# Kernel tuning notes

Measured on AMD Instinct MI355X. Metric: run time of the kernel, lower is better.

The kernel has to match this reference:

```python
import jax, jax.numpy as jnp
import numpy as np

B, T = 2048, 512
H1, H2, H3 = 100, 60, 30


def _glorot(key, shape, fan):
    bound = 1.0 / np.sqrt(fan)
    return jax.random.uniform(key, shape, jnp.float32, -bound, bound)


def setup_inputs() -> dict:
    key = jax.random.key(0)
    ks = jax.random.split(key, 17)
    inp = {"x": jax.random.normal(ks[0], (B, T, 2), jnp.float32)}
    # layer 1: input 2 -> hidden 100
    inp["W_ih1"] = _glorot(ks[1], (H1, 2), H1)
    inp["W_hh1"] = _glorot(ks[2], (H1, H1), H1)
    inp["b_ih1"] = _glorot(ks[3], (H1,), H1)
    inp["b_hh1"] = _glorot(ks[4], (H1,), H1)
    # layer 2: 100 -> 60
    inp["W_ih2"] = _glorot(ks[5], (H2, H1), H2)
    inp["W_hh2"] = _glorot(ks[6], (H2, H2), H2)
    inp["b_ih2"] = _glorot(ks[7], (H2,), H2)
    inp["b_hh2"] = _glorot(ks[8], (H2,), H2)
    # layer 3: 60 -> 30
    inp["W_ih3"] = _glorot(ks[9], (H3, H2), H3)
    inp["W_hh3"] = _glorot(ks[10], (H3, H3), H3)
    inp["b_ih3"] = _glorot(ks[11], (H3,), H3)
    inp["b_hh3"] = _glorot(ks[12], (H3,), H3)
    # heads
    inp["W_o1"] = _glorot(ks[13], (10, H3), 10)
    inp["b_o1"] = _glorot(ks[14], (10,), 10)
    inp["W_o2"] = _glorot(ks[15], (2, 10), 2)
    inp["b_o2"] = _glorot(ks[16], (2,), 2)
    return inp


def rnn_layer(x, W_ih, W_hh, b_ih, b_hh):
    # x: [B, T, in]; precompute the time-parallel input projection once
    xp = jnp.einsum("bti,hi->bth", x, W_ih) + (b_ih + b_hh)  # [B, T, H]
    h0 = jnp.zeros((x.shape[0], W_hh.shape[0]), x.dtype)

    def step(h, xt):  # xt: [B, H]
        h = jnp.tanh(xt + h @ W_hh.T)
        return h, h

    _, ys = jax.lax.scan(step, h0, jnp.swapaxes(xp, 0, 1))  # [T, B, H]
    return jnp.swapaxes(ys, 0, 1)  # [B, T, H]


def reference(x, W_ih1, W_hh1, b_ih1, b_hh1, W_ih2, W_hh2, b_ih2, b_hh2,
              W_ih3, W_hh3, b_ih3, b_hh3, W_o1, b_o1, W_o2, b_o2):
    h = rnn_layer(x, W_ih1, W_hh1, b_ih1, b_hh1)
    h = rnn_layer(h, W_ih2, W_hh2, b_ih2, b_hh2)
    h = rnn_layer(h, W_ih3, W_hh3, b_ih3, b_hh3)
    o = jnp.einsum("bth,oh->bto", h, W_o1) + b_o1
    return jnp.einsum("bto,po->btp", o, W_o2) + b_o2  # [B, T, 2]
```

## Files before the change

### kernel.cpp

```cpp
#include <hip/hip_runtime.h>

typedef _Float16 v8hf __attribute__((ext_vector_type(8)));
typedef float    v4f  __attribute__((ext_vector_type(4)));

#define MFMA16(a, b, c) __builtin_amdgcn_mfma_f32_16x16x32_f16((a), (b), (c), 0, 0, 0)

#define TT 512
#define BT 16
#define NTH 512
#define KS 2.8853900817779268f
#define CL 13.8498724f

#define H1R 0u
#define H2R 8192u
#define XST 12288u
#define ORG 45120u

__shared__ __align__(16) char SM[53312];

__device__ __forceinline__ v4f tanh4s(v4f z) {
    float z0 = __builtin_amdgcn_fmed3f(z[0], -CL, CL);
    float z1 = __builtin_amdgcn_fmed3f(z[1], -CL, CL);
    float z2 = __builtin_amdgcn_fmed3f(z[2], -CL, CL);
    float z3 = __builtin_amdgcn_fmed3f(z[3], -CL, CL);
    float a0 = __builtin_amdgcn_exp2f(z0) + 1.f;
    float a1 = __builtin_amdgcn_exp2f(z1) + 1.f;
    float a2 = __builtin_amdgcn_exp2f(z2) + 1.f;
    float a3 = __builtin_amdgcn_exp2f(z3) + 1.f;
    float P = a0 * a1, Q = a2 * a3;
    float R = __builtin_amdgcn_rcpf(P * Q);
    float iP = Q * R, iQ = P * R;
    v4f t;
    t[0] = 1.f - 2.f * (a1 * iP);
    t[1] = 1.f - 2.f * (a0 * iP);
    t[2] = 1.f - 2.f * (a3 * iQ);
    t[3] = 1.f - 2.f * (a2 * iQ);
    return t;
}

__device__ __forceinline__ unsigned pk2h(float a, float b) {
    union { _Float16 h[2]; unsigned u; } x;
    x.h[0] = (_Float16)a; x.h[1] = (_Float16)b;
    return x.u;
}
__device__ __forceinline__ v8hf mk8(unsigned a, unsigned b, unsigned c, unsigned d) {
    union { unsigned u[4]; v8hf h; } x;
    x.u[0] = a; x.u[1] = b; x.u[2] = c; x.u[3] = d;
    return x.h;
}

__global__ __launch_bounds__(NTH, 1)
void rnn3_sw(const float* __restrict__ xg,
             const float* __restrict__ Wih1, const float* __restrict__ Whh1,
             const float* __restrict__ bih1, const float* __restrict__ bhh1,
             const float* __restrict__ Wih2, const float* __restrict__ Whh2,
             const float* __restrict__ bih2, const float* __restrict__ bhh2,
             const float* __restrict__ Wih3, const float* __restrict__ Whh3,
             const float* __restrict__ bih3, const float* __restrict__ bhh3,
             const float* __restrict__ Wo1,  const float* __restrict__ bo1,
             const float* __restrict__ Wo2,  const float* __restrict__ bo2,
             float* __restrict__ outg)
{
    const int tid   = threadIdx.x;
    const int lane  = tid & 63;
    const int wid   = tid >> 6;
    const int col   = lane & 15;
    const int g     = lane >> 4;
    const int bbase = blockIdx.x * BT;
    const unsigned l16 = (unsigned)lane * 16u;

    {
        float4 z = {0.f, 0.f, 0.f, 0.f};
        for (int i = tid; i < 768; i += NTH) ((float4*)SM)[i] = z;
        for (int i = tid; i < BT * TT; i += NTH) {
            const int b = i >> 9, t = i & 511;
            float2 xv = *(const float2*)(xg + (size_t)(bbase + b) * (TT * 2) + 2 * t);
            *(unsigned*)(SM + XST + (unsigned)t * 64u + (unsigned)b * 4u) = pk2h(xv.x, xv.y);
        }
        if (tid < 16) *(unsigned*)(SM + XST + 512u * 64u + (unsigned)tid * 4u) = 0u;
    }

    v8hf WF[12];
    #pragma unroll
    for (int i = 0; i < 12; ++i) WF[i] = (v8hf)(_Float16)0.f;
    v4f BB0 = {0.f,0.f,0.f,0.f}, BB1 = {0.f,0.f,0.f,0.f}, BH = {0.f,0.f,0.f,0.f};
    v8hf ST = (v8hf)(_Float16)0.f;

    auto ldA = [&](const float* W, int rows, int cols, int jg, int kt) -> v8hf {
        v8hf r;
        #pragma unroll
        for (int e = 0; e < 8; ++e) {
            const int kl = 32 * kt + 16 * (e >> 2) + 4 * g + (e & 3);
            float v = (jg < rows && kl < cols) ? W[jg * cols + kl] * KS : 0.f;
            r[e] = (_Float16)v;
        }
        return r;
    };
    auto ldA1 = [&](int jg, int kt) -> v8hf {
        v8hf r;
        #pragma unroll
        for (int e = 0; e < 8; ++e) {
            const int kl = 32 * kt + 16 * (e >> 2) + 4 * g + (e & 3);
            float v = 0.f;
            if (jg < 100) {
                if (kl < 100)       v = Whh1[jg * 100 + kl];
                else if (kl == 112) v = Wih1[jg * 2];
                else if (kl == 113) v = Wih1[jg * 2 + 1];
            }
            r[e] = (_Float16)(v * KS);
        }
        return r;
    };
    auto mkbias = [&](const float* bi, const float* bh, int n, int t) -> v4f {
        v4f b;
        #pragma unroll
        for (int i = 0; i < 4; ++i) {
            const int j = 16 * t + 4 * g + i;
            b[i] = (j < n) ? KS * (bi[j] + bh[j]) : 0.f;
        }
        return b;
    };

    if (wid < 3) {
        const int tA = 2 * wid;
        #pragma unroll
        for (int kt = 0; kt < 4; ++kt) {
            WF[kt]     = ldA1(16 * tA + col, kt);
            WF[4 + kt] = ldA1(16 * tA + 16 + col, kt);
        }
        BB0 = mkbias(bih1, bhh1, 100, tA);
        BB1 = mkbias(bih1, bhh1, 100, tA + 1);
    } else if (wid == 3) {
        #pragma unroll
        for (int kt = 0; kt < 4; ++kt) WF[kt] = ldA1(96 + col, kt);
        BB0 = mkbias(bih1, bhh1, 100, 6);
    } else if (wid < 6) {
        const int tA = 2 * (wid - 4);
        #pragma unroll
        for (int kt = 0; kt < 4; ++kt) {
            WF[kt]     = ldA(Wih2, 60, 100, 16 * tA + col, kt);
            WF[4 + kt] = ldA(Wih2, 60, 100, 16 * tA + 16 + col, kt);
        }
        WF[8]  = ldA(Whh2, 60, 60, 16 * tA + col, 0);
        WF[9]  = ldA(Whh2, 60, 60, 16 * tA + col, 1);
        WF[10] = ldA(Whh2, 60, 60, 16 * tA + 16 + col, 0);
        WF[11] = ldA(Whh2, 60, 60, 16 * tA + 16 + col, 1);
        BB0 = mkbias(bih2, bhh2, 60, tA);
        BB1 = mkbias(bih2, bhh2, 60, tA + 1);
    } else if (wid == 6) {
        WF[0] = ldA(Wih3, 30, 60, col, 0);       WF[1] = ldA(Wih3, 30, 60, col, 1);
        WF[2] = ldA(Wih3, 30, 60, col + 16, 0);  WF[3] = ldA(Wih3, 30, 60, col + 16, 1);
        WF[4] = ldA(Whh3, 30, 30, col, 0);       WF[5] = ldA(Whh3, 30, 30, col + 16, 0);
        #pragma unroll
        for (int e = 0; e < 8; ++e) {
            const int kl = 16 * (e >> 2) + 4 * g + (e & 3);
            float v = 0.f;
            if (col < 2 && kl < 30) {
                #pragma unroll
                for (int u = 0; u < 10; ++u) v += Wo2[col * 10 + u] * Wo1[u * 30 + kl];
            }
            WF[6][e] = (_Float16)v;
        }
        BB0 = mkbias(bih3, bhh3, 30, 0);
        BB1 = mkbias(bih3, bhh3, 30, 1);
        #pragma unroll
        for (int i = 0; i < 4; ++i) {
            float bv = 0.f;
            if (g == 0 && i < 2) {
                bv = bo2[i];
                #pragma unroll
                for (int u = 0; u < 10; ++u) bv += Wo2[i * 10 + u] * bo1[u];
            }
            BH[i] = bv;
        }
    }

    __syncthreads();
    if (tid < 16)
        *(unsigned*)(SM + H1R + 4096u + 3072u + (unsigned)tid * 16u + 8u) =
            *(const unsigned*)(SM + XST + (unsigned)tid * 4u);
    if (wid == 3) {
        unsigned x0 = *(const unsigned*)(SM + XST + (unsigned)col * 4u);
        ST = mk8(0u, 0u, (g == 0) ? x0 : 0u, 0u);
    }
    __syncthreads();

    auto flushfn = [&](int tbase) {
        const unsigned rb = ORG + (((unsigned)tbase & 63u) >> 1) * 16u;
        #pragma unroll
        for (int jj = 0; jj < 4; ++jj) {
            const int f = lane + 64 * jj;
            const int b = f >> 4, k = f & 15;
            float4 v = *(const float4*)(SM + rb + (unsigned)b * 512u + (unsigned)k * 16u);
            *(float4*)(outg + ((size_t)(bbase + b) * TT + tbase) * 2 + 4 * k) = v;
        }
    };

    unsigned rO1 = H1R + 4096u, wO1 = H1R;
    unsigned rO2 = H2R + 2048u, wO2 = H2R;
    const v4f z4 = {0.f, 0.f, 0.f, 0.f};

    for (int s = 0; s < TT + 2; ++s) {
        if (wid == 0) {
            if (s < TT) {
                v8hf S1 = *(const v8hf*)(SM + rO1 + 1024u + l16);
                v8hf S2 = *(const v8hf*)(SM + rO1 + 2048u + l16);
                v8hf S3 = *(const v8hf*)(SM + rO1 + 3072u + l16);
                v4f p = BB0, q = z4;
                p = MFMA16(WF[0], ST, p); q = MFMA16(WF[1], S1, q);
                p = MFMA16(WF[2], S2, p); q = MFMA16(WF[3], S3, q);
                v4f r0 = tanh4s(p + q);
                p = BB1; q = z4;
                p = MFMA16(WF[4], ST, p); q = MFMA16(WF[5], S1, q);
                p = MFMA16(WF[6], S2, p); q = MFMA16(WF[7], S3, q);
                v4f r1 = tanh4s(p + q);
                ST = mk8(pk2h(r0[0], r0[1]), pk2h(r0[2], r0[3]),
                         pk2h(r1[0], r1[1]), pk2h(r1[2], r1[3]));
                *(v8hf*)(SM + wO1 + l16) = ST;
            }
        } else if (wid == 1) {
            if (s < TT) {
                v8hf S0 = *(const v8hf*)(SM + rO1 + l16);
                v8hf S2 = *(const v8hf*)(SM + rO1 + 2048u + l16);
                v8hf S3 = *(const v8hf*)(SM + rO1 + 3072u + l16);
                v4f p = BB0, q = z4;
                p = MFMA16(WF[0], S0, p); q = MFMA16(WF[1], ST, q);
                p = MFMA16(WF[2], S2, p); q = MFMA16(WF[3], S3, q);
                v4f r0 = tanh4s(p + q);
                p = BB1; q = z4;
                p = MFMA16(WF[4], S0, p); q = MFMA16(WF[5], ST, q);
                p = MFMA16(WF[6], S2, p); q = MFMA16(WF[7], S3, q);
                v4f r1 = tanh4s(p + q);
                ST = mk8(pk2h(r0[0], r0[1]), pk2h(r0[2], r0[3]),
                         pk2h(r1[0], r1[1]), pk2h(r1[2], r1[3]));
                *(v8hf*)(SM + wO1 + 1024u + l16) = ST;
            }
        } else if (wid == 2) {
            if (s < TT) {
                v8hf S0 = *(const v8hf*)(SM + rO1 + l16);
                v8hf S1 = *(const v8hf*)(SM + rO1 + 1024u + l16);
                v8hf S3 = *(const v8hf*)(SM + rO1 + 3072u + l16);
                v4f p = BB0, q = z4;
                p = MFMA16(WF[0], S0, p); q = MFMA16(WF[1], S1, q);
                p = MFMA16(WF[2], ST, p); q = MFMA16(WF[3], S3, q);
                v4f r0 = tanh4s(p + q);
                p = BB1; q = z4;
                p = MFMA16(WF[4], S0, p); q = MFMA16(WF[5], S1, q);
                p = MFMA16(WF[6], ST, p); q = MFMA16(WF[7], S3, q);
                v4f r1 = tanh4s(p + q);
                ST = mk8(pk2h(r0[0], r0[1]), pk2h(r0[2], r0[3]),
                         pk2h(r1[0], r1[1]), pk2h(r1[2], r1[3]));
                *(v8hf*)(SM + wO1 + 2048u + l16) = ST;
            }
        } else if (wid == 3) {
            if (s < TT) {
                v8hf S0 = *(const v8hf*)(SM + rO1 + l16);
                v8hf S1 = *(const v8hf*)(SM + rO1 + 1024u + l16);
                v8hf S2 = *(const v8hf*)(SM + rO1 + 2048u + l16);
                v4f p = BB0, q = z4;
                p = MFMA16(WF[0], S0, p); q = MFMA16(WF[1], S1, q);
                p = MFMA16(WF[2], S2, p); q = MFMA16(WF[3], ST, q);
                v4f r0 = tanh4s(p + q);
                unsigned xn = *(const unsigned*)(SM + XST + (unsigned)(s + 1) * 64u + (unsigned)col * 4u);
                ST = mk8(pk2h(r0[0], r0[1]), pk2h(r0[2], r0[3]),
                         (g == 0) ? xn : 0u, 0u);
                *(v8hf*)(SM + wO1 + 3072u + l16) = ST;
            }
        } else if (wid == 4) {
            if (s >= 1 && s <= TT) {
                v8hf G0 = *(const v8hf*)(SM + rO1 + l16);
                v8hf G1 = *(const v8hf*)(SM + rO1 + 1024u + l16);
                v8hf G2 = *(const v8hf*)(SM + rO1 + 2048u + l16);
                v8hf G3 = *(const v8hf*)(SM + rO1 + 3072u + l16);
                v8hf SB = *(const v8hf*)(SM + rO2 + 1024u + l16);
                v4f p = BB0, q = z4;
                p = MFMA16(WF[0], G0, p); q = MFMA16(WF[1], G1, q);
                p = MFMA16(WF[2], G2, p); q = MFMA16(WF[3], G3, q);
                p = MFMA16(WF[8], ST, p); q = MFMA16(WF[9], SB, q);
                v4f r0 = tanh4s(p + q);
                p = BB1; q = z4;
                p = MFMA16(WF[4], G0, p); q = MFMA16(WF[5], G1, q);
                p = MFMA16(WF[6], G2, p); q = MFMA16(WF[7], G3, q);
                p = MFMA16(WF[10], ST, p); q = MFMA16(WF[11], SB, q);
                v4f r1 = tanh4s(p + q);
                ST = mk8(pk2h(r0[0], r0[1]), pk2h(r0[2], r0[3]),
                         pk2h(r1[0], r1[1]), pk2h(r1[2], r1[3]));
                *(v8hf*)(SM + wO2 + l16) = ST;
            }
        } else if (wid == 5) {
            if (s >= 1 && s <= TT) {
                v8hf G0 = *(const v8hf*)(SM + rO1 + l16);
                v8hf G1 = *(const v8hf*)(SM + rO1 + 1024u + l16);
                v8hf G2 = *(const v8hf*)(SM + rO1 + 2048u + l16);
                v8hf G3 = *(const v8hf*)(SM + rO1 + 3072u + l16);
                v8hf SA = *(const v8hf*)(SM + rO2 + l16);
                v4f p = BB0, q = z4;
                p = MFMA16(WF[0], G0, p); q = MFMA16(WF[1], G1, q);
                p = MFMA16(WF[2], G2, p); q = MFMA16(WF[3], G3, q);
                p = MFMA16(WF[8], SA, p); q = MFMA16(WF[9], ST, q);
                v4f r0 = tanh4s(p + q);
                p = BB1; q = z4;
                p = MFMA16(WF[4], G0, p); q = MFMA16(WF[5], G1, q);
                p = MFMA16(WF[6], G2, p); q = MFMA16(WF[7], G3, q);
                p = MFMA16(WF[10], SA, p); q = MFMA16(WF[11], ST, q);
                v4f r1 = tanh4s(p + q);
                ST = mk8(pk2h(r0[0], r0[1]), pk2h(r0[2], r0[3]),
                         pk2h(r1[0], r1[1]), pk2h(r1[2], r1[3]));
                *(v8hf*)(SM + wO2 + 1024u + l16) = ST;
            }
        } else if (wid == 6) {
            if (s >= 2) {
                v8hf G0 = *(const v8hf*)(SM + rO2 + l16);
                v8hf G1 = *(const v8hf*)(SM + rO2 + 1024u + l16);
                v4f p = BB0, q = z4;
                p = MFMA16(WF[0], G0, p); q = MFMA16(WF[1], G1, q);
                p = MFMA16(WF[4], ST, p);
                v4f r0 = tanh4s(p + q);
                p = BB1; q = z4;
                p = MFMA16(WF[2], G0, p); q = MFMA16(WF[3], G1, q);
                p = MFMA16(WF[5], ST, p);
                v4f r1 = tanh4s(p + q);
                ST = mk8(pk2h(r0[0], r0[1]), pk2h(r0[2], r0[3]),
                         pk2h(r1[0], r1[1]), pk2h(r1[2], r1[3]));
                v4f o = BH;
                o = MFMA16(WF[6], ST, o);
                if (g == 0)
                    *(float2*)(SM + ORG + (unsigned)col * 512u + ((unsigned)(s - 2) & 63u) * 8u) =
                        make_float2(o[0], o[1]);
            }
        } else {
            if (s >= 35 && ((s - 35) & 31) == 0) flushfn(s - 35);
        }
        __syncthreads();
        rO1 ^= 4096u; wO1 ^= 4096u; rO2 ^= 2048u; wO2 ^= 2048u;
    }
    if (wid == 7) flushfn(480);
}

extern "C" void kernel_launch(void* const* d_in, const int* in_sizes, int n_in,
                              void* d_out, int out_size, void* d_ws, size_t ws_size,
                              hipStream_t stream) {
    (void)in_sizes; (void)n_in; (void)d_ws; (void)ws_size; (void)out_size;
    const float* x     = (const float*)d_in[0];
    const float* W_ih1 = (const float*)d_in[1];
    const float* W_hh1 = (const float*)d_in[2];
    const float* b_ih1 = (const float*)d_in[3];
    const float* b_hh1 = (const float*)d_in[4];
    const float* W_ih2 = (const float*)d_in[5];
    const float* W_hh2 = (const float*)d_in[6];
    const float* b_ih2 = (const float*)d_in[7];
    const float* b_hh2 = (const float*)d_in[8];
    const float* W_ih3 = (const float*)d_in[9];
    const float* W_hh3 = (const float*)d_in[10];
    const float* b_ih3 = (const float*)d_in[11];
    const float* b_hh3 = (const float*)d_in[12];
    const float* W_o1  = (const float*)d_in[13];
    const float* b_o1  = (const float*)d_in[14];
    const float* W_o2  = (const float*)d_in[15];
    const float* b_o2  = (const float*)d_in[16];
    float* out = (float*)d_out;

    rnn3_sw<<<2048 / BT, NTH, 0, stream>>>(
        x, W_ih1, W_hh1, b_ih1, b_hh1,
        W_ih2, W_hh2, b_ih2, b_hh2,
        W_ih3, W_hh3, b_ih3, b_hh3,
        W_o1, b_o1, W_o2, b_o2, out);
}
```

Baseline: 333.3 us.

## Split RNN layers across 16 waves with one output tile per wave

Doubles the block to 1024 threads so each wave computes a single 16-row output tile instead of two, removing per-wave register state reuse (ST) in favor of reading all hidden state from shared memory. Layer 3 is split across two waves and the output head gets its own wave, adding a pipeline stage, with a separate wave injecting the next input x. This shortens the serial MFMA and tanh chain per timestep, at the cost of more waves contending at each per-step barrier and an extra pipeline step.

New measurement: 293.3 us. 1.14x faster.

```diff
diff --git a/kernel.cpp b/kernel.cpp
--- a/kernel.cpp
+++ b/kernel.cpp
@@ -7,16 +7,17 @@
 
 #define TT 512
 #define BT 16
-#define NTH 512
+#define NTH 1024
 #define KS 2.8853900817779268f
 #define CL 13.8498724f
 
 #define H1R 0u
 #define H2R 8192u
-#define XST 12288u
-#define ORG 45120u
-
-__shared__ __align__(16) char SM[53312];
+#define H3R 12288u
+#define XST 14336u
+#define ORG 47168u
+
+__shared__ __align__(16) char SM[55360];
 
 __device__ __forceinline__ v4f tanh4s(v4f z) {
     float z0 = __builtin_amdgcn_fmed3f(z[0], -CL, CL);
@@ -43,14 +44,9 @@
     x.h[0] = (_Float16)a; x.h[1] = (_Float16)b;
     return x.u;
 }
-__device__ __forceinline__ v8hf mk8(unsigned a, unsigned b, unsigned c, unsigned d) {
-    union { unsigned u[4]; v8hf h; } x;
-    x.u[0] = a; x.u[1] = b; x.u[2] = c; x.u[3] = d;
-    return x.h;
-}
 
 __global__ __launch_bounds__(NTH, 1)
-void rnn3_sw(const float* __restrict__ xg,
+void rnn3_nu(const float* __restrict__ xg,
              const float* __restrict__ Wih1, const float* __restrict__ Whh1,
              const float* __restrict__ bih1, const float* __restrict__ bhh1,
              const float* __restrict__ Wih2, const float* __restrict__ Whh2,
@@ -71,7 +67,7 @@
 
     {
         float4 z = {0.f, 0.f, 0.f, 0.f};
-        for (int i = tid; i < 768; i += NTH) ((float4*)SM)[i] = z;
+        for (int i = tid; i < 896; i += NTH) ((float4*)SM)[i] = z;
         for (int i = tid; i < BT * TT; i += NTH) {
             const int b = i >> 9, t = i & 511;
             float2 xv = *(const float2*)(xg + (size_t)(bbase + b) * (TT * 2) + 2 * t);
@@ -80,11 +76,10 @@
         if (tid < 16) *(unsigned*)(SM + XST + 512u * 64u + (unsigned)tid * 4u) = 0u;
     }
 
-    v8hf WF[12];
+    v8hf WF[6];
     #pragma unroll
-    for (int i = 0; i < 12; ++i) WF[i] = (v8hf)(_Float16)0.f;
-    v4f BB0 = {0.f,0.f,0.f,0.f}, BB1 = {0.f,0.f,0.f,0.f}, BH = {0.f,0.f,0.f,0.f};
-    v8hf ST = (v8hf)(_Float16)0.f;
+    for (int i = 0; i < 6; ++i) WF[i] = (v8hf)(_Float16)0.f;
+    v4f BB0 = {0.f, 0.f, 0.f, 0.f}, BH = {0.f, 0.f, 0.f, 0.f};
 
     auto ldA = [&](const float* W, int rows, int cols, int jg, int kt) -> v8hf {
         v8hf r;
@@ -121,36 +116,24 @@
         return b;
     };
 
-    if (wid < 3) {
-        const int tA = 2 * wid;
-        #pragma unroll
-        for (int kt = 0; kt < 4; ++kt) {
-            WF[kt]     = ldA1(16 * tA + col, kt);
-            WF[4 + kt] = ldA1(16 * tA + 16 + col, kt);
-        }
-        BB0 = mkbias(bih1, bhh1, 100, tA);
-        BB1 = mkbias(bih1, bhh1, 100, tA + 1);
-    } else if (wid == 3) {
-        #pragma unroll
-        for (int kt = 0; kt < 4; ++kt) WF[kt] = ldA1(96 + col, kt);
-        BB0 = mkbias(bih1, bhh1, 100, 6);
-    } else if (wid < 6) {
-        const int tA = 2 * (wid - 4);
-        #pragma unroll
-        for (int kt = 0; kt < 4; ++kt) {
-            WF[kt]     = ldA(Wih2, 60, 100, 16 * tA + col, kt);
-            WF[4 + kt] = ldA(Wih2, 60, 100, 16 * tA + 16 + col, kt);
-        }
-        WF[8]  = ldA(Whh2, 60, 60, 16 * tA + col, 0);
-        WF[9]  = ldA(Whh2, 60, 60, 16 * tA + col, 1);
-        WF[10] = ldA(Whh2, 60, 60, 16 * tA + 16 + col, 0);
-        WF[11] = ldA(Whh2, 60, 60, 16 * tA + 16 + col, 1);
-        BB0 = mkbias(bih2, bhh2, 60, tA);
-        BB1 = mkbias(bih2, bhh2, 60, tA + 1);
-    } else if (wid == 6) {
-        WF[0] = ldA(Wih3, 30, 60, col, 0);       WF[1] = ldA(Wih3, 30, 60, col, 1);
-        WF[2] = ldA(Wih3, 30, 60, col + 16, 0);  WF[3] = ldA(Wih3, 30, 60, col + 16, 1);
-        WF[4] = ldA(Whh3, 30, 30, col, 0);       WF[5] = ldA(Whh3, 30, 30, col + 16, 0);
+    if (wid < 7) {
+        #pragma unroll
+        for (int kt = 0; kt < 4; ++kt) WF[kt] = ldA1(16 * wid + col, kt);
+        BB0 = mkbias(bih1, bhh1, 100, wid);
+    } else if (wid >= 8 && wid < 12) {
+        const int j = 16 * (wid - 8) + col;
+        #pragma unroll
+        for (int kt = 0; kt < 4; ++kt) WF[kt] = ldA(Wih2, 60, 100, j, kt);
+        WF[4] = ldA(Whh2, 60, 60, j, 0);
+        WF[5] = ldA(Whh2, 60, 60, j, 1);
+        BB0 = mkbias(bih2, bhh2, 60, wid - 8);
+    } else if (wid == 12 || wid == 13) {
+        const int j = 16 * (wid - 12) + col;
+        WF[0] = ldA(Wih3, 30, 60, j, 0);
+        WF[1] = ldA(Wih3, 30, 60, j, 1);
+        WF[2] = ldA(Whh3, 30, 30, j, 0);
+        BB0 = mkbias(bih3, bhh3, 30, wid - 12);
+    } else if (wid == 14) {
         #pragma unroll
         for (int e = 0; e < 8; ++e) {
             const int kl = 16 * (e >> 2) + 4 * g + (e & 3);
@@ -159,10 +142,8 @@
                 #pragma unroll
                 for (int u = 0; u < 10; ++u) v += Wo2[col * 10 + u] * Wo1[u * 30 + kl];
             }
-            WF[6][e] = (_Float16)v;
-        }
-        BB0 = mkbias(bih3, bhh3, 30, 0);
-        BB1 = mkbias(bih3, bhh3, 30, 1);
+            WF[0][e] = (_Float16)v;
+        }
         #pragma unroll
         for (int i = 0; i < 4; ++i) {
             float bv = 0.f;
@@ -179,10 +160,6 @@
     if (tid < 16)
         *(unsigned*)(SM + H1R + 4096u + 3072u + (unsigned)tid * 16u + 8u) =
             *(const unsigned*)(SM + XST + (unsigned)tid * 4u);
-    if (wid == 3) {
-        unsigned x0 = *(const unsigned*)(SM + XST + (unsigned)col * 4u);
-        ST = mk8(0u, 0u, (g == 0) ? x0 : 0u, 0u);
-    }
     __syncthreads();
 
     auto flushfn = [&](int tbase) {
@@ -198,143 +175,85 @@
 
     unsigned rO1 = H1R + 4096u, wO1 = H1R;
     unsigned rO2 = H2R + 2048u, wO2 = H2R;
+    unsigned rO3 = H3R + 1024u, wO3 = H3R;
     const v4f z4 = {0.f, 0.f, 0.f, 0.f};
 
-    for (int s = 0; s < TT + 2; ++s) {
-        if (wid == 0) {
+    for (int s = 0; s < TT + 3; ++s) {
+        if (wid < 7) {
             if (s < TT) {
+                v8hf S0 = *(const v8hf*)(SM + rO1 + l16);
                 v8hf S1 = *(const v8hf*)(SM + rO1 + 1024u + l16);
                 v8hf S2 = *(const v8hf*)(SM + rO1 + 2048u + l16);
                 v8hf S3 = *(const v8hf*)(SM + rO1 + 3072u + l16);
                 v4f p = BB0, q = z4;
-                p = MFMA16(WF[0], ST, p); q = MFMA16(WF[1], S1, q);
+                p = MFMA16(WF[0], S0, p); q = MFMA16(WF[1], S1, q);
                 p = MFMA16(WF[2], S2, p); q = MFMA16(WF[3], S3, q);
-                v4f r0 = tanh4s(p + q);
-                p = BB1; q = z4;
-                p = MFMA16(WF[4], ST, p); q = MFMA16(WF[5], S1, q);
-                p = MFMA16(WF[6], S2, p); q = MFMA16(WF[7], S3, q);
-                v4f r1 = tanh4s(p + q);
-                ST = mk8(pk2h(r0[0], r0[1]), pk2h(r0[2], r0[3]),
-                         pk2h(r1[0], r1[1]), pk2h(r1[2], r1[3]));
-                *(v8hf*)(SM + wO1 + l16) = ST;
-            }
-        } else if (wid == 1) {
-            if (s < TT) {
-                v8hf S0 = *(const v8hf*)(SM + rO1 + l16);
-                v8hf S2 = *(const v8hf*)(SM + rO1 + 2048u + l16);
-                v8hf S3 = *(const v8hf*)(SM + rO1 + 3072u + l16);
-                v4f p = BB0, q = z4;
-                p = MFMA16(WF[0], S0, p); q = MFMA16(WF[1], ST, q);
-                p = MFMA16(WF[2], S2, p); q = MFMA16(WF[3], S3, q);
-                v4f r0 = tanh4s(p + q);
-                p = BB1; q = z4;
-                p = MFMA16(WF[4], S0, p); q = MFMA16(WF[5], ST, q);
-                p = MFMA16(WF[6], S2, p); q = MFMA16(WF[7], S3, q);
-                v4f r1 = tanh4s(p + q);
-                ST = mk8(pk2h(r0[0], r0[1]), pk2h(r0[2], r0[3]),
-                         pk2h(r1[0], r1[1]), pk2h(r1[2], r1[3]));
-                *(v8hf*)(SM + wO1 + 1024u + l16) = ST;
-            }
-        } else if (wid == 2) {
-            if (s < TT) {
-                v8hf S0 = *(const v8hf*)(SM + rO1 + l16);
-                v8hf S1 = *(const v8hf*)(SM + rO1 + 1024u + l16);
-                v8hf S3 = *(const v8hf*)(SM + rO1 + 3072u + l16);
-                v4f p = BB0, q = z4;
-                p = MFMA16(WF[0], S0, p); q = MFMA16(WF[1], S1, q);
-                p = MFMA16(WF[2], ST, p); q = MFMA16(WF[3], S3, q);
-                v4f r0 = tanh4s(p + q);
-                p = BB1; q = z4;
-                p = MFMA16(WF[4], S0, p); q = MFMA16(WF[5], S1, q);
-                p = MFMA16(WF[6], ST, p); q = MFMA16(WF[7], S3, q);
-                v4f r1 = tanh4s(p + q);
-                ST = mk8(pk2h(r0[0], r0[1]), pk2h(r0[2], r0[3]),
-                         pk2h(r1[0], r1[1]), pk2h(r1[2], r1[3]));
-                *(v8hf*)(SM + wO1 + 2048u + l16) = ST;
-            }
-        } else if (wid == 3) {
-            if (s < TT) {
-                v8hf S0 = *(const v8hf*)(SM + rO1 + l16);
-                v8hf S1 = *(const v8hf*)(SM + rO1 + 1024u + l16);
-                v8hf S2 = *(const v8hf*)(SM + rO1 + 2048u + l16);
-                v4f p = BB0, q = z4;
-                p = MFMA16(WF[0], S0, p); q = MFMA16(WF[1], S1, q);
-                p = MFMA16(WF[2], S2, p); q = MFMA16(WF[3], ST, q);
-                v4f r0 = tanh4s(p + q);
-                unsigned xn = *(const unsigned*)(SM + XST + (unsigned)(s + 1) * 64u + (unsigned)col * 4u);
-                ST = mk8(pk2h(r0[0], r0[1]), pk2h(r0[2], r0[3]),
-                         (g == 0) ? xn : 0u, 0u);
-                *(v8hf*)(SM + wO1 + 3072u + l16) = ST;
-            }
-        } else if (wid == 4) {
+                v4f r = tanh4s(p + q);
+                uint2 wv; wv.x = pk2h(r[0], r[1]); wv.y = pk2h(r[2], r[3]);
+                *(uint2*)(SM + wO1 + (unsigned)(wid >> 1) * 1024u + l16
+                             + (unsigned)(wid & 1) * 8u) = wv;
+            }
+        } else if (wid == 7) {
+            if (s < TT - 1) {
+                unsigned xv = *(const unsigned*)(SM + XST + (unsigned)(s + 1) * 64u
+                                                    + (unsigned)col * 4u);
+                uint2 wv; wv.x = (g == 0) ? xv : 0u; wv.y = 0u;
+                *(uint2*)(SM + wO1 + 3072u + l16 + 8u) = wv;
+            }
+        } else if (wid < 12) {
             if (s >= 1 && s <= TT) {
                 v8hf G0 = *(const v8hf*)(SM + rO1 + l16);
                 v8hf G1 = *(const v8hf*)(SM + rO1 + 1024u + l16);
                 v8hf G2 = *(const v8hf*)(SM + rO1 + 2048u + l16);
                 v8hf G3 = *(const v8hf*)(SM + rO1 + 3072u + l16);
-                v8hf SB = *(const v8hf*)(SM + rO2 + 1024u + l16);
-                v4f p = BB0, q = z4;
-                p = MFMA16(WF[0], G0, p); q = MFMA16(WF[1], G1, q);
-                p = MFMA16(WF[2], G2, p); q = MFMA16(WF[3], G3, q);
-                p = MFMA16(WF[8], ST, p); q = MFMA16(WF[9], SB, q);
-                v4f r0 = tanh4s(p + q);
-                p = BB1; q = z4;
-                p = MFMA16(WF[4], G0, p); q = MFMA16(WF[5], G1, q);
-                p = MFMA16(WF[6], G2, p); q = MFMA16(WF[7], G3, q);
-                p = MFMA16(WF[10], ST, p); q = MFMA16(WF[11], SB, q);
-                v4f r1 = tanh4s(p + q);
-                ST = mk8(pk2h(r0[0], r0[1]), pk2h(r0[2], r0[3]),
-                         pk2h(r1[0], r1[1]), pk2h(r1[2], r1[3]));
-                *(v8hf*)(SM + wO2 + l16) = ST;
-            }
-        } else if (wid == 5) {
-            if (s >= 1 && s <= TT) {
-                v8hf G0 = *(const v8hf*)(SM + rO1 + l16);
-                v8hf G1 = *(const v8hf*)(SM + rO1 + 1024u + l16);
-                v8hf G2 = *(const v8hf*)(SM + rO1 + 2048u + l16);
-                v8hf G3 = *(const v8hf*)(SM + rO1 + 3072u + l16);
-                v8hf SA = *(const v8hf*)(SM + rO2 + l16);
-                v4f p = BB0, q = z4;
-                p = MFMA16(WF[0], G0, p); q = MFMA16(WF[1], G1, q);
-                p = MFMA16(WF[2], G2, p); q = MFMA16(WF[3], G3, q);
-                p = MFMA16(WF[8], SA, p); q = MFMA16(WF[9], ST, q);
-                v4f r0 = tanh4s(p + q);
-                p = BB1; q = z4;
-                p = MFMA16(WF[4], G0, p); q = MFMA16(WF[5], G1, q);
-                p = MFMA16(WF[6], G2, p); q = MFMA16(WF[7], G3, q);
-                p = MFMA16(WF[10], SA, p); q = MFMA16(WF[11], ST, q);
-                v4f r1 = tanh4s(p + q);
-                ST = mk8(pk2h(r0[0], r0[1]), pk2h(r0[2], r0[3]),
-                         pk2h(r1[0], r1[1]), pk2h(r1[2], r1[3]));
-                *(v8hf*)(SM + wO2 + 1024u + l16) = ST;
-            }
-        } else if (wid == 6) {
-            if (s >= 2) {
+                v8hf H0 = *(const v8hf*)(SM + rO2 + l16);
+                v8hf H1 = *(const v8hf*)(SM + rO2 + 1024u + l16);
+                v4f p = BB0, q = z4, r2 = z4;
+                p  = MFMA16(WF[0], G0, p);
+                q  = MFMA16(WF[1], G1, q);
+                r2 = MFMA16(WF[4], H0, r2);
+                p  = MFMA16(WF[2], G2, p);
+                q  = MFMA16(WF[3], G3, q);
+                r2 = MFMA16(WF[5], H1, r2);
+                v4f r = tanh4s(p + q + r2);
+                const int t2 = wid - 8;
+                uint2 wv; wv.x = pk2h(r[0], r[1]); wv.y = pk2h(r[2], r[3]);
+                *(uint2*)(SM + wO2 + (unsigned)(t2 >> 1) * 1024u + l16
+                             + (unsigned)(t2 & 1) * 8u) = wv;
+            }
+        } else if (wid < 14) {
+            if (s >= 2 && s <= TT + 1) {
                 v8hf G0 = *(const v8hf*)(SM + rO2 + l16);
                 v8hf G1 = *(const v8hf*)(SM + rO2 + 1024u + l16);
-                v4f p = BB0, q = z4;
-                p = MFMA16(WF[0], G0, p); q = MFMA16(WF[1], G1, q);
-                p = MFMA16(WF[4], ST, p);
-                v4f r0 = tanh4s(p + q);
-                p = BB1; q = z4;
-                p = MFMA16(WF[2], G0, p); q = MFMA16(WF[3], G1, q);
-                p = MFMA16(WF[5], ST, p);
-                v4f r1 = tanh4s(p + q);
-                ST = mk8(pk2h(r0[0], r0[1]), pk2h(r0[2], r0[3]),
-                         pk2h(r1[0], r1[1]), pk2h(r1[2], r1[3]));
+                v8hf C0 = *(const v8hf*)(SM + rO3 + l16);
+                v4f p = BB0, q = z4, r2 = z4;
+                p  = MFMA16(WF[0], G0, p);
+                q  = MFMA16(WF[1], G1, q);
+                r2 = MFMA16(WF[2], C0, r2);
+                v4f r = tanh4s(p + q + r2);
+                const int t3 = wid - 12;
+                uint2 wv; wv.x = pk2h(r[0], r[1]); wv.y = pk2h(r[2], r[3]);
+                *(uint2*)(SM + wO3 + l16 + (unsigned)(t3 & 1) * 8u) = wv;
+            }
+        } else if (wid == 14) {
+            if (s >= 3 && s <= TT + 2) {
+                v8hf C0 = *(const v8hf*)(SM + rO3 + l16);
                 v4f o = BH;
-                o = MFMA16(WF[6], ST, o);
+                o = MFMA16(WF[0], C0, o);
                 if (g == 0)
-                    *(float2*)(SM + ORG + (unsigned)col * 512u + ((unsigned)(s - 2) & 63u) * 8u) =
+                    *(float2*)(SM + ORG + (unsigned)col * 512u
+                                  + ((unsigned)(s - 3) & 63u) * 8u) =
                         make_float2(o[0], o[1]);
             }
         } else {
             if (s >= 35 && ((s - 35) & 31) == 0) flushfn(s - 35);
         }
         __syncthreads();
-        rO1 ^= 4096u; wO1 ^= 4096u; rO2 ^= 2048u; wO2 ^= 2048u;
+        rO1 ^= 4096u; wO1 ^= 4096u;
+        rO2 ^= 2048u; wO2 ^= 2048u;
+        rO3 ^= 1024u; wO3 ^= 1024u;
     }
-    if (wid == 7) flushfn(480);
+    if (wid == 15) flushfn(480);
 }
 
 extern "C" void kernel_launch(void* const* d_in, const int* in_sizes, int n_in,
@@ -360,7 +279,7 @@
     const float* b_o2  = (const float*)d_in[16];
     float* out = (float*)d_out;
 
-    rnn3_sw<<<2048 / BT, NTH, 0, stream>>>(
+    rnn3_nu<<<2048 / BT, NTH, 0, stream>>>(
         x, W_ih1, W_hh1, b_ih1, b_hh1,
         W_ih2, W_hh2, b_ih2, b_hh2,
         W_ih3, W_hh3, b_ih3, b_hh3,
```
